# Performance work log

Measured on AMD Instinct MI355X. Metric: run time of the kernel, lower is better.

The kernel has to match this reference:

```python
import jax, jax.numpy as jnp
import numpy as np
import math

N_FILT = 512
FILT_DIM = 1025
BATCH = 64
FS = 16000.0
FFT_N = 512  # hard-coded n=512 in the original np.fft.rfft call


def setup_inputs() -> dict:
    key = jax.random.key(0)
    kq, = jax.random.split(key, 1)
    # Q factors: positive, realistic filter quality factors in [2, 10)
    Q = jax.random.uniform(kq, (BATCH, N_FILT), dtype=jnp.float32) * 8.0 + 2.0
    # center frequencies exactly as the module computes f_cos:
    # fdelta = fs/2/N_filt; fc = arange(fdelta/2, fs/2, fdelta)
    fdelta = FS / 2.0 / N_FILT
    fc = jnp.asarray(np.arange(fdelta / 2.0, FS / 2.0, fdelta), dtype=jnp.float32)
    return {"Q": Q, "fc": fc}


def reference(Q, fc):
    # Q: [B, F] quality factors, fc: [F] center frequencies (Hz)
    T = FILT_DIM - 1
    # nT = t_right * fs = [1, 2, ..., N-1]
    n = jnp.arange(1, T + 1, dtype=Q.dtype)                      # [T]
    BW = fc[None, :] / Q                                         # [B, F]
    alpha = BW * (0.5 * math.sqrt(2.0 * math.pi))                # [B, F]
    b = alpha / FS                                               # [B, F]
    omega_c = (2.0 * math.pi / FS) * fc                          # [F]
    # y[b,f,t] = exp(-(b*n)^2) * cos(omega_c * n)
    env = jnp.exp(-jnp.square(b[:, :, None] * n))                # [B, F, T]
    carrier = jnp.cos(omega_c[None, :, None] * n)                # [1, F, T] bcast
    y = env * carrier                                            # [B, F, T]
    # per-filter max |rfft| over batch and frequency bins (detached in original)
    fft_mag = jnp.abs(jnp.fft.rfft(y, n=FFT_N, axis=-1))         # [B, F, 257]
    maxfft = jax.lax.stop_gradient(jnp.max(fft_mag, axis=(0, 2)))  # [F]
    filters = jnp.flip(y / maxfft[None, :, None], axis=-1)       # [B, F, T]
    return filters
```

## Files before the change

### kernel.cpp

```cpp
#include <hip/hip_runtime.h>


#define BCOEF_K 7.8332133582218756e-05f
#define INV_FS  6.25e-05f
#define TWO_PI  6.28318530717958647692f
#define PI_F    3.14159265358979323846f
#define SIGK_K  115.2309f
#define KAPPA   1.3f
#define FULL_FC 700.0f

typedef float vf4 __attribute__((ext_vector_type(4)));

__device__ __forceinline__ float fast_carrier(float fcn, float n) {
  float rev = fcn * n;
  float fr  = rev - floorf(rev);
  return __cosf(TWO_PI * fr);
}
__device__ __forceinline__ float fast_env(float x) { return __expf(-x * x); }

__global__ __launch_bounds__(256) void k_maxfft(const float* __restrict__ Q,
                                                const float* __restrict__ fc,
                                                float* __restrict__ ws) {
  const int tid  = threadIdx.x;
  const int w    = tid >> 6;
  const int lane = tid & 63;
  const int sig  = blockIdx.x * 4 + w;
  const int f    = sig & 511;
  const int bb   = sig >> 9;

  __shared__ __align__(16) float ybuf[4][512];

  const float fcv = fc[f];
  const float q   = Q[bb * 512 + f];
  const float bc  = (fcv / q) * BCOEF_K;
  const float fcn = fcv * INV_FS;

  float qq = Q[lane * 512 + f];
  #pragma unroll
  for (int d = 32; d > 0; d >>= 1) qq = fmaxf(qq, __shfl_xor(qq, d));
  if (fcv >= FULL_FC && bc * qq > KAPPA * fcv * BCOEF_K) {
    if (lane == 0) ws[f * 64 + bb] = 0.0f;
    return;
  }

  const float nstar = 4.0f / bc;
  const int   N_eff = (nstar >= 510.0f) ? 512 : ((int)nstar + 2);
  const int   jmax  = (N_eff + 3) >> 2;
  const int   n4    = jmax << 2;

  float* yw = &ybuf[w][0];
  const int nit_g = (n4 + 63) >> 6;
  for (int r = 0; r < nit_g; ++r) {
    const int idx = (r << 6) + lane;
    const float n = (float)(idx + 1);
    const float v = fast_env(bc * n) * fast_carrier(fcn, n);
    if (idx < n4) yw[idx] = v;
  }
  asm volatile("s_waitcnt lgkmcnt(0)" ::: "memory");

  const int kci  = (int)(fcn * 512.0f + 0.5f);
  const int W    = (int)(2.0f * (bc * SIGK_K)) + 6;
  const int k_lo = max(0, kci - W);
  const int k_hi = min(256, kci + W);
  const int nit  = ((k_hi - k_lo) >> 6) + 1;

  const float4* y4 = (const float4*)yw;
  float mx = 0.0f;
  for (int it = 0; it < nit; ++it) {
    const int   k = min(k_lo + (it << 6) + lane, k_hi);
    const float c = 2.0f * cosf((float)k * (PI_F / 256.0f));
    float s1 = 0.0f, s2 = 0.0f;
    #pragma unroll 4
    for (int j = 0; j < jmax; ++j) {
      const float4 x = y4[j];
      float s;
      s = fmaf(c, s1, x.x - s2); s2 = s1; s1 = s;
      s = fmaf(c, s1, x.y - s2); s2 = s1; s1 = s;
      s = fmaf(c, s1, x.z - s2); s2 = s1; s1 = s;
      s = fmaf(c, s1, x.w - s2); s2 = s1; s1 = s;
    }
    mx = fmaxf(mx, fmaf(s1, s1, fmaf(s2, s2, -(c * s1 * s2))));
  }

  #pragma unroll
  for (int d = 32; d > 0; d >>= 1) mx = fmaxf(mx, __shfl_xor(mx, d));
  if (lane == 0) ws[f * 64 + bb] = mx;
}

__global__ __launch_bounds__(256) void k_write(const float* __restrict__ Q,
                                               const float* __restrict__ fc,
                                               const float* __restrict__ ws,
                                               float* __restrict__ out) {
  const int tid  = threadIdx.x;
  const int w    = tid >> 6;
  const int lane = tid & 63;
  const int sig  = blockIdx.x * 4 + w;
  const int f    = sig & 511;
  const int bb   = sig >> 9;

  float mx = ws[f * 64 + lane];
  #pragma unroll
  for (int d = 32; d > 0; d >>= 1) mx = fmaxf(mx, __shfl_xor(mx, d));
  const float inv = rsqrtf(mx);

  const float fcv = fc[f];
  const float q   = Q[bb * 512 + f];
  const float bc  = (fcv / q) * BCOEF_K;
  const float fcn = fcv * INV_FS;
  const float nstar = 4.0f / bc;

  vf4* __restrict__ orow = (vf4*)out + (size_t)sig * 256;
  #pragma unroll
  for (int r = 0; r < 4; ++r) {
    const int qi = (r << 6) + lane;
    const int t0 = qi << 2;
    vf4 v = {0.0f, 0.0f, 0.0f, 0.0f};
    if ((float)(1021 - t0) <= nstar) {
      const float n0 = (float)(1024 - t0);
      const float n1 = (float)(1023 - t0);
      const float n2 = (float)(1022 - t0);
      const float n3 = (float)(1021 - t0);
      v.x = fast_env(bc * n0) * fast_carrier(fcn, n0) * inv;
      v.y = fast_env(bc * n1) * fast_carrier(fcn, n1) * inv;
      v.z = fast_env(bc * n2) * fast_carrier(fcn, n2) * inv;
      v.w = fast_env(bc * n3) * fast_carrier(fcn, n3) * inv;
    }
    orow[qi] = v;
  }
}

extern "C" void kernel_launch(void* const* d_in, const int* in_sizes, int n_in,
                              void* d_out, int out_size, void* d_ws, size_t ws_size,
                              hipStream_t stream) {
  const float* Q  = (const float*)d_in[0];
  const float* fc = (const float*)d_in[1];
  float* out      = (float*)d_out;
  float* ws       = (float*)d_ws;

  k_maxfft<<<64 * 512 / 4, 256, 0, stream>>>(Q, fc, ws);
  k_write <<<64 * 512 / 4, 256, 0, stream>>>(Q, fc, ws, out);
}
```

Measured before the change: 159.4 us.

## Fuse max-FFT and write kernels into one per-filter block

Replaces the two-kernel scheme (per-signal max-FFT to workspace, then normalize-and-write) with a single kernel where each block handles one filter across all 64 batch entries. Eight waves loop over batches, reduce the max in shared memory, then write the normalized outputs. This removes a kernel launch and the global workspace round trip. The cost is only 512 blocks, which gives less parallelism and possible load imbalance since batch entries differ in work.

```diff
diff --git a/kernel.cpp b/kernel.cpp
--- a/kernel.cpp
+++ b/kernel.cpp
@@ -18,114 +18,107 @@
 }
 __device__ __forceinline__ float fast_env(float x) { return __expf(-x * x); }
 
-__global__ __launch_bounds__(256) void k_maxfft(const float* __restrict__ Q,
+__global__ __launch_bounds__(512) void k_filter(const float* __restrict__ Q,
                                                 const float* __restrict__ fc,
-                                                float* __restrict__ ws) {
+                                                float* __restrict__ out) {
   const int tid  = threadIdx.x;
   const int w    = tid >> 6;
   const int lane = tid & 63;
-  const int sig  = blockIdx.x * 4 + w;
-  const int f    = sig & 511;
-  const int bb   = sig >> 9;
+  const int f    = blockIdx.x;
 
-  __shared__ __align__(16) float ybuf[4][512];
+  __shared__ __align__(16) float ybuf[8][512];
+  __shared__ float smax[64];
 
   const float fcv = fc[f];
-  const float q   = Q[bb * 512 + f];
-  const float bc  = (fcv / q) * BCOEF_K;
   const float fcn = fcv * INV_FS;
 
   float qq = Q[lane * 512 + f];
   #pragma unroll
   for (int d = 32; d > 0; d >>= 1) qq = fmaxf(qq, __shfl_xor(qq, d));
-  if (fcv >= FULL_FC && bc * qq > KAPPA * fcv * BCOEF_K) {
-    if (lane == 0) ws[f * 64 + bb] = 0.0f;
-    return;
+
+  float* const yw = &ybuf[w][0];
+  const float4* const y4 = (const float4*)yw;
+
+  for (int i = 0; i < 8; ++i) {
+    const int   bb = (i << 3) + w;
+    const float q  = Q[bb * 512 + f];
+    const float bc = (fcv / q) * BCOEF_K;
+    float mx = 0.0f;
+
+    if (!(fcv >= FULL_FC && bc * qq > KAPPA * fcv * BCOEF_K)) {
+      const float nstar = 4.0f / bc;
+      const int   N_eff = (nstar >= 510.0f) ? 512 : ((int)nstar + 2);
+      const int   jmax  = (N_eff + 3) >> 2;
+      const int   n4    = jmax << 2;
+
+      asm volatile("s_waitcnt lgkmcnt(0)" ::: "memory");
+
+      const int nit_g = (n4 + 63) >> 6;
+      for (int r = 0; r < nit_g; ++r) {
+        const int idx = (r << 6) + lane;
+        const float n = (float)(idx + 1);
+        const float v = fast_env(bc * n) * fast_carrier(fcn, n);
+        if (idx < n4) yw[idx] = v;
+      }
+      asm volatile("s_waitcnt lgkmcnt(0)" ::: "memory");
+
+      const int kci  = (int)(fcn * 512.0f + 0.5f);
+      const int W    = (int)(2.0f * (bc * SIGK_K)) + 6;
+      const int k_lo = max(0, kci - W);
+      const int k_hi = min(256, kci + W);
+      const int nit  = ((k_hi - k_lo) >> 6) + 1;
+
+      for (int it = 0; it < nit; ++it) {
+        const int   k = min(k_lo + (it << 6) + lane, k_hi);
+        const float c = 2.0f * cosf((float)k * (PI_F / 256.0f));
+        float s1 = 0.0f, s2 = 0.0f;
+        #pragma unroll 4
+        for (int j = 0; j < jmax; ++j) {
+          const float4 x = y4[j];
+          float s;
+          s = fmaf(c, s1, x.x - s2); s2 = s1; s1 = s;
+          s = fmaf(c, s1, x.y - s2); s2 = s1; s1 = s;
+          s = fmaf(c, s1, x.z - s2); s2 = s1; s1 = s;
+          s = fmaf(c, s1, x.w - s2); s2 = s1; s1 = s;
+        }
+        mx = fmaxf(mx, fmaf(s1, s1, fmaf(s2, s2, -(c * s1 * s2))));
+      }
+      #pragma unroll
+      for (int d = 32; d > 0; d >>= 1) mx = fmaxf(mx, __shfl_xor(mx, d));
+    }
+    if (lane == 0) smax[bb] = mx;
   }
 
-  const float nstar = 4.0f / bc;
-  const int   N_eff = (nstar >= 510.0f) ? 512 : ((int)nstar + 2);
-  const int   jmax  = (N_eff + 3) >> 2;
-  const int   n4    = jmax << 2;
+  __syncthreads();
 
-  float* yw = &ybuf[w][0];
-  const int nit_g = (n4 + 63) >> 6;
-  for (int r = 0; r < nit_g; ++r) {
-    const int idx = (r << 6) + lane;
-    const float n = (float)(idx + 1);
-    const float v = fast_env(bc * n) * fast_carrier(fcn, n);
-    if (idx < n4) yw[idx] = v;
-  }
-  asm volatile("s_waitcnt lgkmcnt(0)" ::: "memory");
+  float mxall = smax[lane];
+  #pragma unroll
+  for (int d = 32; d > 0; d >>= 1) mxall = fmaxf(mxall, __shfl_xor(mxall, d));
+  const float inv = rsqrtf(mxall);
 
-  const int kci  = (int)(fcn * 512.0f + 0.5f);
-  const int W    = (int)(2.0f * (bc * SIGK_K)) + 6;
-  const int k_lo = max(0, kci - W);
-  const int k_hi = min(256, kci + W);
-  const int nit  = ((k_hi - k_lo) >> 6) + 1;
-
-  const float4* y4 = (const float4*)yw;
-  float mx = 0.0f;
-  for (int it = 0; it < nit; ++it) {
-    const int   k = min(k_lo + (it << 6) + lane, k_hi);
-    const float c = 2.0f * cosf((float)k * (PI_F / 256.0f));
-    float s1 = 0.0f, s2 = 0.0f;
-    #pragma unroll 4
-    for (int j = 0; j < jmax; ++j) {
-      const float4 x = y4[j];
-      float s;
-      s = fmaf(c, s1, x.x - s2); s2 = s1; s1 = s;
-      s = fmaf(c, s1, x.y - s2); s2 = s1; s1 = s;
-      s = fmaf(c, s1, x.z - s2); s2 = s1; s1 = s;
-      s = fmaf(c, s1, x.w - s2); s2 = s1; s1 = s;
+  for (int i = 0; i < 8; ++i) {
+    const int   bb = (i << 3) + w;
+    const float q  = Q[bb * 512 + f];
+    const float bc = (fcv / q) * BCOEF_K;
+    const float ns = 4.0f / bc;
+    vf4* __restrict__ orow = (vf4*)out + (size_t)(bb * 512 + f) * 256;
+    #pragma unroll
+    for (int r = 0; r < 4; ++r) {
+      const int qi = (r << 6) + lane;
+      const int t0 = qi << 2;
+      vf4 v = {0.0f, 0.0f, 0.0f, 0.0f};
+      if ((float)(1021 - t0) <= ns) {
+        const float n0 = (float)(1024 - t0);
+        const float n1 = (float)(1023 - t0);
+        const float n2 = (float)(1022 - t0);
+        const float n3 = (float)(1021 - t0);
+        v.x = fast_env(bc * n0) * fast_carrier(fcn, n0) * inv;
+        v.y = fast_env(bc * n1) * fast_carrier(fcn, n1) * inv;
+        v.z = fast_env(bc * n2) * fast_carrier(fcn, n2) * inv;
+        v.w = fast_env(bc * n3) * fast_carrier(fcn, n3) * inv;
+      }
+      orow[qi] = v;
     }
-    mx = fmaxf(mx, fmaf(s1, s1, fmaf(s2, s2, -(c * s1 * s2))));
-  }
-
-  #pragma unroll
-  for (int d = 32; d > 0; d >>= 1) mx = fmaxf(mx, __shfl_xor(mx, d));
-  if (lane == 0) ws[f * 64 + bb] = mx;
-}
-
-__global__ __launch_bounds__(256) void k_write(const float* __restrict__ Q,
-                                               const float* __restrict__ fc,
-                                               const float* __restrict__ ws,
-                                               float* __restrict__ out) {
-  const int tid  = threadIdx.x;
-  const int w    = tid >> 6;
-  const int lane = tid & 63;
-  const int sig  = blockIdx.x * 4 + w;
-  const int f    = sig & 511;
-  const int bb   = sig >> 9;
-
-  float mx = ws[f * 64 + lane];
-  #pragma unroll
-  for (int d = 32; d > 0; d >>= 1) mx = fmaxf(mx, __shfl_xor(mx, d));
-  const float inv = rsqrtf(mx);
-
-  const float fcv = fc[f];
-  const float q   = Q[bb * 512 + f];
-  const float bc  = (fcv / q) * BCOEF_K;
-  const float fcn = fcv * INV_FS;
-  const float nstar = 4.0f / bc;
-
-  vf4* __restrict__ orow = (vf4*)out + (size_t)sig * 256;
-  #pragma unroll
-  for (int r = 0; r < 4; ++r) {
-    const int qi = (r << 6) + lane;
-    const int t0 = qi << 2;
-    vf4 v = {0.0f, 0.0f, 0.0f, 0.0f};
-    if ((float)(1021 - t0) <= nstar) {
-      const float n0 = (float)(1024 - t0);
-      const float n1 = (float)(1023 - t0);
-      const float n2 = (float)(1022 - t0);
-      const float n3 = (float)(1021 - t0);
-      v.x = fast_env(bc * n0) * fast_carrier(fcn, n0) * inv;
-      v.y = fast_env(bc * n1) * fast_carrier(fcn, n1) * inv;
-      v.z = fast_env(bc * n2) * fast_carrier(fcn, n2) * inv;
-      v.w = fast_env(bc * n3) * fast_carrier(fcn, n3) * inv;
-    }
-    orow[qi] = v;
   }
 }
 
@@ -135,8 +128,7 @@
   const float* Q  = (const float*)d_in[0];
   const float* fc = (const float*)d_in[1];
   float* out      = (float*)d_out;
-  float* ws       = (float*)d_ws;
+  (void)d_ws; (void)ws_size;
 
-  k_maxfft<<<64 * 512 / 4, 256, 0, stream>>>(Q, fc, ws);
-  k_write <<<64 * 512 / 4, 256, 0, stream>>>(Q, fc, ws, out);
+  k_filter<<<512, 512, 0, stream>>>(Q, fc, out);
 }
```

Result: slower. 165.9 us (+4.1%).

## Pack four batch signals per wave in maxfft, sharing lanes across full-length Goertzel rows

Applied to the files above, without the earlier changes.

The max-FFT kernel now gives each wave four batch entries of the same filter instead of one, and launches a quarter as many blocks. Signals that need the full 512-sample Goertzel run are processed together: each 16-lane group handles one signal, so the mostly idle lanes of narrow-band filters share a single pass over LDS. Other signals still go through the old per-signal path, run one after another within the wave. This cuts wasted lanes and repeated sequential Goertzel loops, but raises LDS use per block and serialises the non-full signals inside each wave.

```diff
diff --git a/kernel.cpp b/kernel.cpp
--- a/kernel.cpp
+++ b/kernel.cpp
@@ -18,73 +18,147 @@
 }
 __device__ __forceinline__ float fast_env(float x) { return __expf(-x * x); }
 
-__global__ __launch_bounds__(256) void k_maxfft(const float* __restrict__ Q,
-                                                const float* __restrict__ fc,
-                                                float* __restrict__ ws) {
-  const int tid  = threadIdx.x;
-  const int w    = tid >> 6;
-  const int lane = tid & 63;
-  const int sig  = blockIdx.x * 4 + w;
-  const int f    = sig & 511;
-  const int bb   = sig >> 9;
-
-  __shared__ __align__(16) float ybuf[4][512];
+#define ROWF 516
+
+__global__ __launch_bounds__(256) void k_maxfft2(const float* __restrict__ Q,
+                                                 const float* __restrict__ fc,
+                                                 float* __restrict__ ws) {
+  const int tid   = threadIdx.x;
+  const int w     = tid >> 6;
+  const int lane  = tid & 63;
+  const int f     = blockIdx.x & 511;
+  const int chunk = blockIdx.x >> 9;
+  const int bb0   = chunk * 16 + w * 4;
+
+  __shared__ __align__(16) float ybuf[4][4][ROWF];
+  float* const rows = &ybuf[w][0][0];
 
   const float fcv = fc[f];
-  const float q   = Q[bb * 512 + f];
-  const float bc  = (fcv / q) * BCOEF_K;
   const float fcn = fcv * INV_FS;
+  const int   kci = (int)(fcn * 512.0f + 0.5f);
 
   float qq = Q[lane * 512 + f];
   #pragma unroll
   for (int d = 32; d > 0; d >>= 1) qq = fmaxf(qq, __shfl_xor(qq, d));
-  if (fcv >= FULL_FC && bc * qq > KAPPA * fcv * BCOEF_K) {
-    if (lane == 0) ws[f * 64 + bb] = 0.0f;
-    return;
-  }
-
-  const float nstar = 4.0f / bc;
-  const int   N_eff = (nstar >= 510.0f) ? 512 : ((int)nstar + 2);
-  const int   jmax  = (N_eff + 3) >> 2;
-  const int   n4    = jmax << 2;
-
-  float* yw = &ybuf[w][0];
-  const int nit_g = (n4 + 63) >> 6;
-  for (int r = 0; r < nit_g; ++r) {
-    const int idx = (r << 6) + lane;
-    const float n = (float)(idx + 1);
-    const float v = fast_env(bc * n) * fast_carrier(fcn, n);
-    if (idx < n4) yw[idx] = v;
-  }
-  asm volatile("s_waitcnt lgkmcnt(0)" ::: "memory");
-
-  const int kci  = (int)(fcn * 512.0f + 0.5f);
-  const int W    = (int)(2.0f * (bc * SIGK_K)) + 6;
-  const int k_lo = max(0, kci - W);
-  const int k_hi = min(256, kci + W);
-  const int nit  = ((k_hi - k_lo) >> 6) + 1;
-
-  const float4* y4 = (const float4*)yw;
-  float mx = 0.0f;
-  for (int it = 0; it < nit; ++it) {
-    const int   k = min(k_lo + (it << 6) + lane, k_hi);
-    const float c = 2.0f * cosf((float)k * (PI_F / 256.0f));
+  const float prthr = KAPPA * fcv * BCOEF_K;
+
+  const float q0 = Q[(bb0 + 0) * 512 + f];
+  const float q1 = Q[(bb0 + 1) * 512 + f];
+  const float q2 = Q[(bb0 + 2) * 512 + f];
+  const float q3 = Q[(bb0 + 3) * 512 + f];
+  const float bc0 = (fcv / q0) * BCOEF_K;
+  const float bc1 = (fcv / q1) * BCOEF_K;
+  const float bc2 = (fcv / q2) * BCOEF_K;
+  const float bc3 = (fcv / q3) * BCOEF_K;
+  const bool pr0 = (fcv >= FULL_FC && bc0 * qq > prthr);
+  const bool pr1 = (fcv >= FULL_FC && bc1 * qq > prthr);
+  const bool pr2 = (fcv >= FULL_FC && bc2 * qq > prthr);
+  const bool pr3 = (fcv >= FULL_FC && bc3 * qq > prthr);
+  const bool fl0 = !pr0 && (4.0f / bc0 >= 510.0f);
+  const bool fl1 = !pr1 && (4.0f / bc1 >= 510.0f);
+  const bool fl2 = !pr2 && (4.0f / bc2 >= 510.0f);
+  const bool fl3 = !pr3 && (4.0f / bc3 >= 510.0f);
+  const int firstFL = fl0 ? 0 : fl1 ? 1 : fl2 ? 2 : fl3 ? 3 : -1;
+
+  if (firstFL >= 0) {
+    #define GENROW(g, bcg)                                                    \
+      {                                                                       \
+        float* yr = rows + (g) * ROWF;                                        \
+        _Pragma("unroll")                                                     \
+        for (int r = 0; r < 8; ++r) {                                         \
+          const int idx = (r << 6) + lane;                                    \
+          const float n = (float)(idx + 1);                                   \
+          yr[idx] = fast_env((bcg) * n) * fast_carrier(fcn, n);               \
+        }                                                                     \
+      }
+    if (fl0) GENROW(0, bc0)
+    if (fl1) GENROW(1, bc1)
+    if (fl2) GENROW(2, bc2)
+    if (fl3) GENROW(3, bc3)
+    #undef GENROW
+    asm volatile("s_waitcnt lgkmcnt(0)" ::: "memory");
+
+    const int g = lane >> 4;
+    const int l = lane & 15;
+    const bool flg = (g == 0) ? fl0 : (g == 1) ? fl1 : (g == 2) ? fl2 : fl3;
+    const int  gsel = flg ? g : firstFL;
+    const float bcg = (gsel == 0) ? bc0 : (gsel == 1) ? bc1
+                    : (gsel == 2) ? bc2 : bc3;
+    const float4* const y4g = (const float4*)(rows + gsel * ROWF);
+
+    const int W    = (int)(2.0f * (bcg * SIGK_K)) + 6;
+    const int k_lo = max(0, kci - W);
+    const int k_hi = min(256, kci + W);
+    const int k    = min(k_lo + l, k_hi);
+    const float c  = 2.0f * cosf((float)k * (PI_F / 256.0f));
+
     float s1 = 0.0f, s2 = 0.0f;
     #pragma unroll 4
-    for (int j = 0; j < jmax; ++j) {
-      const float4 x = y4[j];
+    for (int j = 0; j < 128; ++j) {
+      const float4 x = y4g[j];
       float s;
       s = fmaf(c, s1, x.x - s2); s2 = s1; s1 = s;
       s = fmaf(c, s1, x.y - s2); s2 = s1; s1 = s;
       s = fmaf(c, s1, x.z - s2); s2 = s1; s1 = s;
       s = fmaf(c, s1, x.w - s2); s2 = s1; s1 = s;
     }
-    mx = fmaxf(mx, fmaf(s1, s1, fmaf(s2, s2, -(c * s1 * s2))));
+    float mx = fmaxf(0.0f, fmaf(s1, s1, fmaf(s2, s2, -(c * s1 * s2))));
+    #pragma unroll
+    for (int d = 8; d > 0; d >>= 1) mx = fmaxf(mx, __shfl_xor(mx, d));
+    if (l == 0 && flg) ws[f * 64 + (bb0 + g)] = mx;
   }
 
-  #pragma unroll
-  for (int d = 32; d > 0; d >>= 1) mx = fmaxf(mx, __shfl_xor(mx, d));
-  if (lane == 0) ws[f * 64 + bb] = mx;
+  #define SERIAL(j, bcj, prj, flj)                                            \
+    {                                                                         \
+      if (prj) {                                                              \
+        if (lane == 0) ws[f * 64 + (bb0 + (j))] = 0.0f;                       \
+      } else if (!(flj)) {                                                    \
+        const float bc = (bcj);                                               \
+        const float nstar = 4.0f / bc;                                        \
+        const int   N_eff = (nstar >= 510.0f) ? 512 : ((int)nstar + 2);       \
+        const int   jmax  = (N_eff + 3) >> 2;                                 \
+        const int   n4    = jmax << 2;                                        \
+        float* yw = rows + (j) * ROWF;                                        \
+        asm volatile("s_waitcnt lgkmcnt(0)" ::: "memory");                    \
+        const int nit_g = (n4 + 63) >> 6;                                     \
+        for (int r = 0; r < nit_g; ++r) {                                     \
+          const int idx = (r << 6) + lane;                                    \
+          const float n = (float)(idx + 1);                                   \
+          const float v = fast_env(bc * n) * fast_carrier(fcn, n);            \
+          if (idx < n4) yw[idx] = v;                                          \
+        }                                                                     \
+        asm volatile("s_waitcnt lgkmcnt(0)" ::: "memory");                    \
+        const int W    = (int)(2.0f * (bc * SIGK_K)) + 6;                     \
+        const int k_lo = max(0, kci - W);                                     \
+        const int k_hi = min(256, kci + W);                                   \
+        const int nit  = ((k_hi - k_lo) >> 6) + 1;                            \
+        const float4* y4 = (const float4*)yw;                                 \
+        float mx = 0.0f;                                                      \
+        for (int it = 0; it < nit; ++it) {                                    \
+          const int   k = min(k_lo + (it << 6) + lane, k_hi);                 \
+          const float c = 2.0f * cosf((float)k * (PI_F / 256.0f));            \
+          float s1 = 0.0f, s2 = 0.0f;                                         \
+          _Pragma("unroll 4")                                                 \
+          for (int jj = 0; jj < jmax; ++jj) {                                 \
+            const float4 x = y4[jj];                                          \
+            float s;                                                          \
+            s = fmaf(c, s1, x.x - s2); s2 = s1; s1 = s;                       \
+            s = fmaf(c, s1, x.y - s2); s2 = s1; s1 = s;                       \
+            s = fmaf(c, s1, x.z - s2); s2 = s1; s1 = s;                       \
+            s = fmaf(c, s1, x.w - s2); s2 = s1; s1 = s;                       \
+          }                                                                   \
+          mx = fmaxf(mx, fmaf(s1, s1, fmaf(s2, s2, -(c * s1 * s2))));         \
+        }                                                                     \
+        _Pragma("unroll")                                                     \
+        for (int d = 32; d > 0; d >>= 1) mx = fmaxf(mx, __shfl_xor(mx, d));   \
+        if (lane == 0) ws[f * 64 + (bb0 + (j))] = mx;                         \
+      }                                                                       \
+    }
+  SERIAL(0, bc0, pr0, fl0)
+  SERIAL(1, bc1, pr1, fl1)
+  SERIAL(2, bc2, pr2, fl2)
+  SERIAL(3, bc3, pr3, fl3)
+  #undef SERIAL
 }
 
 __global__ __launch_bounds__(256) void k_write(const float* __restrict__ Q,
@@ -137,6 +211,6 @@
   float* out      = (float*)d_out;
   float* ws       = (float*)d_ws;
 
-  k_maxfft<<<64 * 512 / 4, 256, 0, stream>>>(Q, fc, ws);
-  k_write <<<64 * 512 / 4, 256, 0, stream>>>(Q, fc, ws, out);
-}
+  k_maxfft2<<<2048,       256, 0, stream>>>(Q, fc, ws);
+  k_write  <<<64 * 512 / 4, 256, 0, stream>>>(Q, fc, ws, out);
+}
```

New measurement: 159.8 us. About the same (+0.3%).
